# Kernel tuning notes

Hardware: AMD Instinct MI355X
Metric: run time of the kernel (lower is better)

Reference implementation:

```python
import jax, jax.numpy as jnp
import numpy as np
from jax import lax

# dims (see shape_source)
B, C, H, W = 2, 128, 48, 48
HEADS = 4
G = 4                 # offset_groups = heads
DH = C // HEADS       # 32, dim_head
DF = 4                # downsample_factor
OKS = 6               # offset_kernel_size
PAD = (OKS - DF) // 2 # 1
OFFSET_SCALE = 4.0
CPB_DIM = C // 4      # 32
OD = C // G           # offset_dims = 32


def setup_inputs() -> dict:
    key = jax.random.key(0)
    ks = jax.random.split(key, 12)
    rn = lambda k, shape, s=0.05: jax.random.normal(k, shape, dtype=jnp.float32) * s
    return {
        "x": jax.random.normal(ks[0], (B, C, H, W), dtype=jnp.float32),
        "gamma": jax.random.normal(ks[1], (1,), dtype=jnp.float32),  # nn.Parameter([0.0]); randomized so both paths contribute
        "wq": rn(ks[2], (G, DH, C // G)),    # grouped 1x1 conv, groups=G
        "wk": rn(ks[3], (G, DH, C // G)),
        "wv": rn(ks[4], (G, DH, C // G)),
        "wo": rn(ks[5], (C, C)),             # to_out 1x1 conv
        "bo": jnp.zeros((C,), jnp.float32),
        "w_off_dw": rn(ks[6], (OD, 1, OKS, OKS)),  # depthwise conv k=6 s=4 p=1
        "b_off_dw": jnp.zeros((OD,), jnp.float32),
        "w_off_proj": rn(ks[7], (2, OD)),          # 1x1 conv to 2 offset channels, no bias
        "cpb_w0": rn(ks[8], (2, CPB_DIM), 0.5),
        "cpb_b0": jnp.zeros((CPB_DIM,), jnp.float32),
        "cpb_w1": rn(ks[9], (CPB_DIM, CPB_DIM), 0.2),
        "cpb_b1": jnp.zeros((CPB_DIM,), jnp.float32),
        "cpb_w2": rn(ks[10], (CPB_DIM, HEADS // G), 0.2),
        "cpb_b2": jnp.zeros((HEADS // G,), jnp.float32),
    }


def _bilinear_sample(img, px, py):
    """F.grid_sample(mode='bilinear', padding_mode='zeros') on pixel coords.
    img: (N, Cg, Hi, Wi); px, py: (N, Ho, Wo) -> (N, Cg, Ho, Wo)"""
    N, Cg, Hi, Wi = img.shape
    imgf = img.reshape(N, Cg, Hi * Wi)
    x0 = jnp.floor(px)
    y0 = jnp.floor(py)
    wx1 = px - x0
    wy1 = py - y0

    def corner(xc, yc, w):
        valid = (xc >= 0) & (xc <= Wi - 1) & (yc >= 0) & (yc <= Hi - 1)
        xi = jnp.clip(xc, 0, Wi - 1).astype(jnp.int32)
        yi = jnp.clip(yc, 0, Hi - 1).astype(jnp.int32)
        idx = (yi * Wi + xi).reshape(N, -1)
        vals = jnp.take_along_axis(imgf, idx[:, None, :], axis=2)  # (N,Cg,Ho*Wo)
        return vals * (w * valid).reshape(N, 1, -1)

    out = (corner(x0, y0, (1 - wx1) * (1 - wy1))
           + corner(x0 + 1, y0, wx1 * (1 - wy1))
           + corner(x0, y0 + 1, (1 - wx1) * wy1)
           + corner(x0 + 1, y0 + 1, wx1 * wy1))
    return out.reshape(N, Cg, px.shape[1], px.shape[2])


def _forward(x, gamma, wq, wk, wv, wo, bo, w_off_dw, b_off_dw, w_off_proj,
             cpb_w0, cpb_b0, cpb_w1, cpb_b1, cpb_w2, cpb_b2):
    b = x.shape[0]
    scale = DH ** -0.5
    xg = x.reshape(b, G, C // G, H, W)
    # grouped 1x1 conv -> queries (b, G, DH, H, W); channel layout (g d) == (h d) since G==HEADS
    q = jnp.einsum('bgchw,goc->bgohw', xg, wq)
    gq = q.reshape(b * G, DH, H, W)
    # to_offsets: depthwise conv (k=6, s=4, p=1) -> GELU -> 1x1 to 2ch -> tanh -> *offset_scale
    off = lax.conv_general_dilated(gq, w_off_dw, (DF, DF), [(PAD, PAD), (PAD, PAD)],
                                   feature_group_count=OD,
                                   dimension_numbers=('NCHW', 'OIHW', 'NCHW'))
    off = jax.nn.gelu(off + b_off_dw[None, :, None, None], approximate=False)
    off = jnp.tanh(jnp.einsum('bchw,oc->bohw', off, w_off_proj)) * OFFSET_SCALE  # (bG,2,Hd,Wd)
    Hd, Wd = off.shape[-2], off.shape[-1]
    gy, gx = jnp.meshgrid(jnp.arange(Hd, dtype=jnp.float32),
                          jnp.arange(Wd, dtype=jnp.float32), indexing='ij')
    vg0 = gx[None] + off[:, 0]  # channel 0 = x (meshgrid 'xy' in torch code)
    vg1 = gy[None] + off[:, 1]  # channel 1 = y
    vn0 = 2.0 * vg0 / max(Hd - 1, 1) - 1.0  # normalize_grid (H==W so h/w quirk is moot)
    vn1 = 2.0 * vg1 / max(Wd - 1, 1) - 1.0
    # grid_sample align_corners=False unnormalization: pix = ((u+1)*size - 1)/2
    px = ((vn0 + 1.0) * W - 1.0) / 2.0
    py = ((vn1 + 1.0) * H - 1.0) / 2.0
    kv = _bilinear_sample(xg.reshape(b * G, C // G, H, W), px, py)  # (bG, C/G, Hd, Wd)
    kvg = kv.reshape(b, G, C // G, Hd, Wd)
    k = jnp.einsum('bgchw,goc->bgohw', kvg, wk)
    v = jnp.einsum('bgchw,goc->bgohw', kvg, wv)
    i, j = H * W, Hd * Wd
    qh = q.reshape(b, HEADS, DH, i).transpose(0, 1, 3, 2) * scale  # (b,h,i,d)
    kh = k.reshape(b, HEADS, DH, j).transpose(0, 1, 3, 2)
    vh = v.reshape(b, HEADS, DH, j).transpose(0, 1, 3, 2)
    sim = jnp.einsum('bhid,bhjd->bhij', qh, kh)
    # CPB relative position bias
    gyq, gxq = jnp.meshgrid(jnp.arange(H, dtype=jnp.float32),
                            jnp.arange(W, dtype=jnp.float32), indexing='ij')
    qn0 = 2.0 * gxq / max(H - 1, 1) - 1.0
    qn1 = 2.0 * gyq / max(W - 1, 1) - 1.0
    grid_q = jnp.stack([qn0, qn1], -1).reshape(1, i, 1, 2)
    grid_kv = jnp.stack([vn0, vn1], -1).reshape(b * G, 1, j, 2)
    pos = grid_q - grid_kv                       # (bG, i, j, 2)
    bias = jnp.sign(pos) * jnp.log1p(jnp.abs(pos))
    h1 = jax.nn.relu(bias @ cpb_w0 + cpb_b0)
    h2 = jax.nn.relu(h1 @ cpb_w1 + cpb_b1)
    bias = h2 @ cpb_w2 + cpb_b2                  # (bG, i, j, heads//G)
    bias = bias.reshape(b, G, i, j, HEADS // G).transpose(0, 1, 4, 2, 3).reshape(b, HEADS, i, j)
    attn = jax.nn.softmax(sim + bias, axis=-1)
    outh = jnp.einsum('bhij,bhjd->bhid', attn, vh)
    out = outh.transpose(0, 1, 3, 2).reshape(b, C, H, W)  # 'b h (x y) d -> b (h d) x y'
    attention = jnp.einsum('bchw,oc->bohw', out, wo) + bo[None, :, None, None]
    return gamma[0] * attention + x, attention


def reference(x, gamma, wq, wk, wv, wo, bo, w_off_dw, b_off_dw, w_off_proj,
              cpb_w0, cpb_b0, cpb_w1, cpb_b1, cpb_w2, cpb_b2):
    return _forward(x, gamma, wq, wk, wv, wo, bo, w_off_dw, b_off_dw, w_off_proj,
                    cpb_w0, cpb_b0, cpb_w1, cpb_b1, cpb_w2, cpb_b2)
```

## Files before the change

### kernel.cpp

```cpp
#include <hip/hip_runtime.h>
#include <math.h>

#define HWHW 2304
#define JD   144
#define LSP  148

typedef __attribute__((ext_vector_type(8))) short short8;
typedef __attribute__((ext_vector_type(4))) float f32x4;

__device__ inline ushort f2bf(float f) {
  uint u = __float_as_uint(f);
  u += 0x7fffu + ((u >> 16) & 1u);
  return (ushort)(u >> 16);
}
__device__ inline float bf2f(ushort s) { return __uint_as_float((uint)s << 16); }


__global__ __launch_bounds__(256) void qproj_kernel(
    const float* __restrict__ x, const float* __restrict__ wq,
    ushort* __restrict__ qt) {
  int hw = blockIdx.x * 256 + threadIdx.x;
  int o0 = blockIdx.y * 8, bg = blockIdx.z;
  int b = bg >> 2, g = bg & 3;
  const float* xp = x + (b * 128 + g * 32) * HWHW + hw;
  float xv[32];
#pragma unroll
  for (int c = 0; c < 32; ++c) xv[c] = xp[c * HWHW];
  uint p[4];
#pragma unroll
  for (int oo = 0; oo < 8; oo += 2) {
    const float* w0r = wq + (g * 32 + o0 + oo) * 32;
    const float* w1r = wq + (g * 32 + o0 + oo + 1) * 32;
    float a0 = 0.f, a1 = 0.f;
#pragma unroll
    for (int c = 0; c < 32; ++c) { a0 += w0r[c] * xv[c]; a1 += w1r[c] * xv[c]; }
    p[oo >> 1] = (uint)f2bf(a0) | ((uint)f2bf(a1) << 16);
  }
  *(uint4*)(qt + ((long)bg * HWHW + hw) * 32 + o0) = make_uint4(p[0], p[1], p[2], p[3]);
}

__global__ __launch_bounds__(384) void offset_kv_kernel(
    const ushort* __restrict__ qt, const float* __restrict__ wdw,
    const float* __restrict__ bdw, const float* __restrict__ wproj,
    const float* __restrict__ x, const float* __restrict__ wk,
    const float* __restrict__ wv,
    float* __restrict__ vn0, float* __restrict__ vn1,
    ushort* __restrict__ ktb, ushort* __restrict__ vtb) {
  __shared__ float qs[288][32];
  __shared__ float wdws[36][32];
  __shared__ float wkl[32][33], wvl[32][33];
  __shared__ float kvs[32][13];
  __shared__ float spx[12], spy[12];
  int hd = blockIdx.x, bg = blockIdx.y, b = bg >> 2, g = bg & 3;
  int t = threadIdx.x;
  for (int u = t; u < 4608; u += 384) {
    int r = u >> 4, c2 = u & 15;
    int ry = r / 48, col = r - ry * 48;
    int hy = hd * 4 - 1 + ry;
    uint v = 0;
    if (hy >= 0 && hy < 48)
      v = ((const uint*)qt)[((long)bg * HWHW + hy * 48 + col) * 16 + c2];
    qs[r][c2 * 2] = bf2f((ushort)v);
    qs[r][c2 * 2 + 1] = bf2f((ushort)(v >> 16));
  }
  for (int u = t; u < 1152; u += 384) wdws[u >> 5][u & 31] = wdw[(u & 31) * 36 + (u >> 5)];
  for (int u = t; u < 1024; u += 384) {
    int d = u >> 5, c = u & 31;
    wkl[d][c] = wk[g * 1024 + u];
    wvl[d][c] = wv[g * 1024 + u];
  }
  __syncthreads();
  {
    int wd = t >> 5, c = t & 31;
    float s = 0.f;
#pragma unroll
    for (int ky = 0; ky < 6; ++ky) {
#pragma unroll
      for (int kx = 0; kx < 6; ++kx) {
        int wx = wd * 4 - 1 + kx;
        if (wx >= 0 && wx < 48)
          s += wdws[ky * 6 + kx][c] * qs[ky * 48 + wx][c];
      }
    }
    s += bdw[c];
    s = 0.5f * s * (1.f + erff(s * 0.70710678118654752f));
    float g0 = wproj[c] * s;
    float g1 = wproj[32 + c] * s;
#pragma unroll
    for (int k = 16; k >= 1; k >>= 1) {
      g0 += __shfl_xor(g0, k, 64);
      g1 += __shfl_xor(g1, k, 64);
    }
    if (c == 0) {
      float off0 = tanhf(g0) * 4.f;
      float off1 = tanhf(g1) * 4.f;
      float n0 = 2.f * ((float)wd + off0) / 11.f - 1.f;
      float n1 = 2.f * ((float)hd + off1) / 11.f - 1.f;
      int idx = bg * JD + hd * 12 + wd;
      vn0[idx] = n0;
      vn1[idx] = n1;
      spx[wd] = ((n0 + 1.f) * 48.f - 1.f) * 0.5f;
      spy[wd] = ((n1 + 1.f) * 48.f - 1.f) * 0.5f;
    }
  }
  __syncthreads();
  {
    int j = t >> 5, c = t & 31;
    float fx = spx[j], fy = spy[j];
    float x0 = floorf(fx), y0 = floorf(fy);
    float wx = fx - x0, wy = fy - y0;
    int xi = (int)x0, yi = (int)y0;
    const float* xp = x + (b * 128 + g * 32 + c) * HWHW;
    float v00 = 0.f, v10 = 0.f, v01 = 0.f, v11 = 0.f;
    bool okx0 = (xi >= 0) & (xi < 48), okx1 = (xi + 1 >= 0) & (xi + 1 < 48);
    if (yi >= 0 && yi < 48) {
      if (okx0) v00 = xp[yi * 48 + xi];
      if (okx1) v10 = xp[yi * 48 + xi + 1];
    }
    if (yi + 1 >= 0 && yi + 1 < 48) {
      if (okx0) v01 = xp[(yi + 1) * 48 + xi];
      if (okx1) v11 = xp[(yi + 1) * 48 + xi + 1];
    }
    kvs[c][j] = v00 * (1.f - wx) * (1.f - wy) + v10 * wx * (1.f - wy)
              + v01 * (1.f - wx) * wy + v11 * wx * wy;
  }
  __syncthreads();
  {
    int j = t >> 5, d = t & 31;
    float ak = 0.f, av = 0.f;
#pragma unroll
    for (int c = 0; c < 32; ++c) {
      float val = kvs[c][j];
      ak += wkl[d][c] * val;
      av += wvl[d][c] * val;
    }
    int jg = hd * 12 + j;
    ktb[bg * 4608 + jg * 32 + d] = f2bf(ak);
    vtb[bg * 5120 + d * 160 + jg] = f2bf(av);
  }
  if (hd == 0) {
    for (int u = t; u < 512; u += 384)
      vtb[bg * 5120 + (u >> 4) * 160 + 144 + (u & 15)] = 0;
  }
}

__global__ __launch_bounds__(256) void attn_fused_kernel(
    const ushort* __restrict__ qt, const ushort* __restrict__ ktb,
    const ushort* __restrict__ vtb,
    const float* __restrict__ vn0, const float* __restrict__ vn1,
    const float* __restrict__ w0, const float* __restrict__ b0,
    const float* __restrict__ w1, const float* __restrict__ b1,
    const float* __restrict__ w2, const float* __restrict__ b2,
    ushort* __restrict__ outh) {
  __shared__ __align__(16) char smem[21888];
  float* Ls = (float*)smem;
  ushort* kbf = (ushort*)(smem + 9472);
  ushort* vbfT = (ushort*)(smem + 9472);
  ushort* qbf = (ushort*)(smem + 19712);
  float* sv0 = (float*)(smem + 20736);
  float* sv1 = (float*)(smem + 21312);

  int bg = blockIdx.y, b = bg >> 2, g = bg & 3;
  int i0 = blockIdx.x * 16;
  int t = threadIdx.x;
  int w = t >> 6, lane = t & 63;
  int lam = lane & 15, quad = lane >> 4;

  {
    const uint4* src = (const uint4*)(ktb + bg * 4608);
    uint4* dst = (uint4*)kbf;
    for (int u = t; u < 576; u += 256) dst[u] = src[u];
    if (t < 128) ((uint4*)qbf)[t & 127] =
        ((const uint4*)(qt + ((long)bg * HWHW + i0) * 32))[t & 127];
  }
  if (t < JD) { sv0[t] = vn0[bg * JD + t]; sv1[t] = vn1[bg * JD + t]; }

  float w00r[8], w01r[8], b0r[8];
#pragma unroll
  for (int j = 0; j < 8; ++j) {
    int k = quad * 8 + j;
    w00r[j] = w0[k]; w01r[j] = w0[32 + k]; b0r[j] = b0[k];
  }
  short8 w1f0, w1f1;
#pragma unroll
  for (int j = 0; j < 8; ++j) {
    int k = quad * 8 + j;
    w1f0[j] = (short)f2bf(w1[k * 32 + lam]);
    w1f1[j] = (short)f2bf(w1[k * 32 + 16 + lam]);
  }
  f32x4 zA, zB;
  float w2r[8];
#pragma unroll
  for (int r = 0; r < 4; ++r) {
    zA[r] = b1[quad * 4 + r];
    zB[r] = b1[16 + quad * 4 + r];
    w2r[r] = w2[quad * 4 + r];
    w2r[4 + r] = w2[16 + quad * 4 + r];
  }
  float b2s = b2[0];

  __syncthreads();

  const float scale = 0.17677669529663687f;
  {
    short8 aq = *(const short8*)(qbf + lam * 32 + quad * 8);
#pragma unroll 1
    for (int jt = w; jt < 9; jt += 4) {
      short8 bk = *(const short8*)(kbf + (jt * 16 + lam) * 32 + quad * 8);
      f32x4 acc = {0.f, 0.f, 0.f, 0.f};
      acc = __builtin_amdgcn_mfma_f32_16x16x32_bf16(aq, bk, acc, 0, 0, 0);
#pragma unroll
      for (int r = 0; r < 4; ++r)
        Ls[(quad * 4 + r) * LSP + jt * 16 + lam] = acc[r] * scale;
    }
  }
  __syncthreads();

#pragma unroll 1
  for (int s = 0; s < 9; ++s) {
    int P = s * 64 + lane;
    int ii = P / 144, jj = P - ii * 144;
    int ig = i0 + w * 4 + ii;
    int iy = ig / 48, ix = ig - iy * 48;
    float p0 = (float)ix * (2.f / 47.f) - 1.f - sv0[jj];
    float p1 = (float)iy * (2.f / 47.f) - 1.f - sv1[jj];
    float s0f = copysignf(__logf(1.f + fabsf(p0)), p0);
    float s1f = copysignf(__logf(1.f + fabsf(p1)), p1);
    float bm[4];
#pragma unroll
    for (int mt = 0; mt < 4; ++mt) {
      float s0 = __shfl(s0f, mt * 16 + lam, 64);
      float s1 = __shfl(s1f, mt * 16 + lam, 64);
      float h[8];
#pragma unroll
      for (int j = 0; j < 8; ++j)
        h[j] = fmaxf(fmaf(s0, w00r[j], fmaf(s1, w01r[j], b0r[j])), 0.f);
      union { uint u[4]; short8 s8; } cvt;
#pragma unroll
      for (int j = 0; j < 4; ++j)
        cvt.u[j] = __builtin_amdgcn_perm(__float_as_uint(h[2 * j + 1]),
                                         __float_as_uint(h[2 * j]), 0x07060302);
      f32x4 dA = __builtin_amdgcn_mfma_f32_16x16x32_bf16(w1f0, cvt.s8, zA, 0, 0, 0);
      f32x4 dB = __builtin_amdgcn_mfma_f32_16x16x32_bf16(w1f1, cvt.s8, zB, 0, 0, 0);
      float acc = 0.f;
#pragma unroll
      for (int r = 0; r < 4; ++r) {
        acc = fmaf(fmaxf(dA[r], 0.f), w2r[r], acc);
        acc = fmaf(fmaxf(dB[r], 0.f), w2r[4 + r], acc);
      }
      acc += __shfl_xor(acc, 16, 64);
      acc += __shfl_xor(acc, 32, 64);
      bm[mt] = acc;
    }
    float biasv = (quad == 0 ? bm[0] : quad == 1 ? bm[1] : quad == 2 ? bm[2] : bm[3]) + b2s;
    Ls[(w * 4 + ii) * LSP + jj] += biasv;
  }
  __syncthreads();

  {
    const uint4* src = (const uint4*)(vtb + bg * 5120);
    uint4* dst = (uint4*)vbfT;
    for (int u = t; u < 640; u += 256) dst[u] = src[u];
  }

#pragma unroll 1
  for (int rr = 0; rr < 4; ++rr) {
    int row = w * 4 + rr;
    const float* Lp = Ls + row * LSP;
    float l0 = Lp[lane], l1 = Lp[64 + lane];
    float l2 = (lane < 16) ? Lp[128 + lane] : -INFINITY;
    float m = fmaxf(fmaxf(l0, l1), l2);
#pragma unroll
    for (int k = 32; k >= 1; k >>= 1) m = fmaxf(m, __shfl_xor(m, k, 64));
    float e0 = __expf(l0 - m), e1 = __expf(l1 - m);
    float e2 = (lane < 16) ? __expf(l2 - m) : 0.f;
    float sum = e0 + e1 + e2;
#pragma unroll
    for (int k = 32; k >= 1; k >>= 1) sum += __shfl_xor(sum, k, 64);
    float inv = 1.f / sum;
    ushort* pb = (ushort*)(Lp + 64);
    pb[lane] = f2bf(e0 * inv);
    pb[64 + lane] = f2bf(e1 * inv);
    if (lane < 32) pb[128 + lane] = (lane < 16) ? f2bf(e2 * inv) : (ushort)0;
  }
  __syncthreads();

  if (w < 2) {
    f32x4 o = {0.f, 0.f, 0.f, 0.f};
    const ushort* pb = (const ushort*)(Ls + lam * LSP + 64);
    const ushort* vb = vbfT + (w * 16 + lam) * 160;
#pragma unroll
    for (int kb = 0; kb < 5; ++kb) {
      short8 ap = *(const short8*)(pb + kb * 32 + quad * 8);
      short8 bv = *(const short8*)(vb + kb * 32 + quad * 8);
      o = __builtin_amdgcn_mfma_f32_16x16x32_bf16(ap, bv, o, 0, 0, 0);
    }
#pragma unroll
    for (int r = 0; r < 4; ++r) {
      int ig = i0 + quad * 4 + r;
      outh[((long)b * HWHW + ig) * 128 + g * 32 + w * 16 + lam] = f2bf(o[r]);
    }
  }
}

__global__ __launch_bounds__(256) void out_kernel(
    const ushort* __restrict__ outh, const float* __restrict__ wo,
    const float* __restrict__ bo, const float* __restrict__ x,
    const float* __restrict__ gamma, float* __restrict__ out) {
  __shared__ __align__(16) char smem[39168];
  ushort* wob = (ushort*)smem;
  ushort* aob = (ushort*)(smem + 34816);
  int b = blockIdx.y;
  int hw0 = blockIdx.x * 16;
  int t = threadIdx.x;
  int w = t >> 6, lane = t & 63, lam = lane & 15, quad = lane >> 4;
  {
    const float2* wsrc = (const float2*)wo;
    for (int u = t; u < 8192; u += 256) {
      float2 v = wsrc[u];
      ((uint*)wob)[(u >> 6) * 68 + (u & 63)] =
          (uint)f2bf(v.x) | ((uint)f2bf(v.y) << 16);
    }
  }
  {
    const uint* src = (const uint*)(outh + ((long)b * HWHW + hw0) * 128);
    for (int u = t; u < 1024; u += 256)
      ((uint*)aob)[(u >> 6) * 68 + (u & 63)] = src[u];
  }
  __syncthreads();
  f32x4 acc0 = {0.f, 0.f, 0.f, 0.f}, acc1 = {0.f, 0.f, 0.f, 0.f};
#pragma unroll
  for (int ks = 0; ks < 4; ++ks) {
    short8 a = *(const short8*)(aob + lam * 136 + ks * 32 + quad * 8);
    short8 b0f = *(const short8*)(wob + (w * 32 + lam) * 136 + ks * 32 + quad * 8);
    short8 b1f = *(const short8*)(wob + (w * 32 + 16 + lam) * 136 + ks * 32 + quad * 8);
    acc0 = __builtin_amdgcn_mfma_f32_16x16x32_bf16(a, b0f, acc0, 0, 0, 0);
    acc1 = __builtin_amdgcn_mfma_f32_16x16x32_bf16(a, b1f, acc1, 0, 0, 0);
  }
  float gm = gamma[0];
  float* out0 = out;
  float* out1 = out + 2 * 128 * HWHW;
#pragma unroll
  for (int nt = 0; nt < 2; ++nt) {
    f32x4 acc = nt ? acc1 : acc0;
    int oc = w * 32 + nt * 16 + lam;
    float bv = bo[oc];
    long base = ((long)(b * 128 + oc)) * HWHW + hw0 + quad * 4;
    float4 xv = *(const float4*)(x + base);
    float4 a1, a0;
    a1.x = acc[0] + bv; a1.y = acc[1] + bv; a1.z = acc[2] + bv; a1.w = acc[3] + bv;
    a0.x = fmaf(gm, a1.x, xv.x); a0.y = fmaf(gm, a1.y, xv.y);
    a0.z = fmaf(gm, a1.z, xv.z); a0.w = fmaf(gm, a1.w, xv.w);
    *(float4*)(out1 + base) = a1;
    *(float4*)(out0 + base) = a0;
  }
}

extern "C" void kernel_launch(void* const* d_in, const int* in_sizes, int n_in,
                              void* d_out, int out_size, void* d_ws, size_t ws_size,
                              hipStream_t stream) {
  const float* x     = (const float*)d_in[0];
  const float* gamma = (const float*)d_in[1];
  const float* wq    = (const float*)d_in[2];
  const float* wk    = (const float*)d_in[3];
  const float* wv    = (const float*)d_in[4];
  const float* wo    = (const float*)d_in[5];
  const float* bo    = (const float*)d_in[6];
  const float* wdw   = (const float*)d_in[7];
  const float* bdw   = (const float*)d_in[8];
  const float* wproj = (const float*)d_in[9];
  const float* cw0   = (const float*)d_in[10];
  const float* cb0   = (const float*)d_in[11];
  const float* cw1   = (const float*)d_in[12];
  const float* cb1   = (const float*)d_in[13];
  const float* cw2   = (const float*)d_in[14];
  const float* cb2   = (const float*)d_in[15];
  char* wsb = (char*)d_ws;
  ushort* qt  = (ushort*)wsb;
  float* vn0  = (float*)(wsb + 1179648);
  float* vn1  = (float*)(wsb + 1184256);
  ushort* ktb = (ushort*)(wsb + 1188864);
  ushort* vtb = (ushort*)(wsb + 1262592);
  ushort* outh = (ushort*)(wsb + 1344512);
  float* out  = (float*)d_out;

  qproj_kernel<<<dim3(9, 4, 8), 256, 0, stream>>>(x, wq, qt);
  offset_kv_kernel<<<dim3(12, 8), 384, 0, stream>>>(qt, wdw, bdw, wproj, x, wk, wv,
                                                    vn0, vn1, ktb, vtb);
  attn_fused_kernel<<<dim3(144, 8), 256, 0, stream>>>(qt, ktb, vtb, vn0, vn1,
                                                      cw0, cb0, cw1, cb1, cw2, cb2, outh);
  out_kernel<<<dim3(144, 2), 256, 0, stream>>>(outh, wo, bo, x, gamma, out);
}
```

Before: 138.0 us.

## Load MFMA operands directly from global memory instead of staging in LDS

The attention kernel no longer copies Q, K and V tiles into shared memory. It reads the MFMA fragments straight from global memory, which shrinks its LDS footprint and drops one barrier. The output projection kernel drops its shared-memory staging of the full wo matrix and the activation tile. It now loads fp32 weights per fragment and packs them to bf16 by truncation instead of round-to-nearest. This removes the redundant per-block conversion and copy of wo and should raise occupancy, at the cost of more uncoalesced global and L2 reads and a small rounding change.

Result: no change. 135.6 us (-1.7%).

```diff
diff --git a/kernel.cpp b/kernel.cpp
--- a/kernel.cpp
+++ b/kernel.cpp
@@ -14,6 +14,9 @@
   return (ushort)(u >> 16);
 }
 __device__ inline float bf2f(ushort s) { return __uint_as_float((uint)s << 16); }
+__device__ inline uint packbf(float hi, float lo) {
+  return __builtin_amdgcn_perm(__float_as_uint(hi), __float_as_uint(lo), 0x07060302);
+}
 
 
 __global__ __launch_bounds__(256) void qproj_kernel(
@@ -152,13 +155,10 @@
     const float* __restrict__ w1, const float* __restrict__ b1,
     const float* __restrict__ w2, const float* __restrict__ b2,
     ushort* __restrict__ outh) {
-  __shared__ __align__(16) char smem[21888];
+  __shared__ __align__(16) char smem[10624];
   float* Ls = (float*)smem;
-  ushort* kbf = (ushort*)(smem + 9472);
-  ushort* vbfT = (ushort*)(smem + 9472);
-  ushort* qbf = (ushort*)(smem + 19712);
-  float* sv0 = (float*)(smem + 20736);
-  float* sv1 = (float*)(smem + 21312);
+  float* sv0 = (float*)(smem + 9472);
+  float* sv1 = (float*)(smem + 10048);
 
   int bg = blockIdx.y, b = bg >> 2, g = bg & 3;
   int i0 = blockIdx.x * 16;
@@ -166,13 +166,6 @@
   int w = t >> 6, lane = t & 63;
   int lam = lane & 15, quad = lane >> 4;
 
-  {
-    const uint4* src = (const uint4*)(ktb + bg * 4608);
-    uint4* dst = (uint4*)kbf;
-    for (int u = t; u < 576; u += 256) dst[u] = src[u];
-    if (t < 128) ((uint4*)qbf)[t & 127] =
-        ((const uint4*)(qt + ((long)bg * HWHW + i0) * 32))[t & 127];
-  }
   if (t < JD) { sv0[t] = vn0[bg * JD + t]; sv1[t] = vn1[bg * JD + t]; }
 
   float w00r[8], w01r[8], b0r[8];
@@ -199,14 +192,13 @@
   }
   float b2s = b2[0];
 
-  __syncthreads();
-
   const float scale = 0.17677669529663687f;
   {
-    short8 aq = *(const short8*)(qbf + lam * 32 + quad * 8);
+    short8 aq = *(const short8*)(qt + ((long)bg * HWHW + i0 + lam) * 32 + quad * 8);
+    const ushort* kb = ktb + bg * 4608;
 #pragma unroll 1
     for (int jt = w; jt < 9; jt += 4) {
-      short8 bk = *(const short8*)(kbf + (jt * 16 + lam) * 32 + quad * 8);
+      short8 bk = *(const short8*)(kb + (jt * 16 + lam) * 32 + quad * 8);
       f32x4 acc = {0.f, 0.f, 0.f, 0.f};
       acc = __builtin_amdgcn_mfma_f32_16x16x32_bf16(aq, bk, acc, 0, 0, 0);
 #pragma unroll
@@ -237,9 +229,7 @@
         h[j] = fmaxf(fmaf(s0, w00r[j], fmaf(s1, w01r[j], b0r[j])), 0.f);
       union { uint u[4]; short8 s8; } cvt;
 #pragma unroll
-      for (int j = 0; j < 4; ++j)
-        cvt.u[j] = __builtin_amdgcn_perm(__float_as_uint(h[2 * j + 1]),
-                                         __float_as_uint(h[2 * j]), 0x07060302);
+      for (int j = 0; j < 4; ++j) cvt.u[j] = packbf(h[2 * j + 1], h[2 * j]);
       f32x4 dA = __builtin_amdgcn_mfma_f32_16x16x32_bf16(w1f0, cvt.s8, zA, 0, 0, 0);
       f32x4 dB = __builtin_amdgcn_mfma_f32_16x16x32_bf16(w1f1, cvt.s8, zB, 0, 0, 0);
       float acc = 0.f;
@@ -257,12 +247,6 @@
   }
   __syncthreads();
 
-  {
-    const uint4* src = (const uint4*)(vtb + bg * 5120);
-    uint4* dst = (uint4*)vbfT;
-    for (int u = t; u < 640; u += 256) dst[u] = src[u];
-  }
-
 #pragma unroll 1
   for (int rr = 0; rr < 4; ++rr) {
     int row = w * 4 + rr;
@@ -288,7 +272,7 @@
   if (w < 2) {
     f32x4 o = {0.f, 0.f, 0.f, 0.f};
     const ushort* pb = (const ushort*)(Ls + lam * LSP + 64);
-    const ushort* vb = vbfT + (w * 16 + lam) * 160;
+    const ushort* vb = vtb + bg * 5120 + (w * 16 + lam) * 160;
 #pragma unroll
     for (int kb = 0; kb < 5; ++kb) {
       short8 ap = *(const short8*)(pb + kb * 32 + quad * 8);
@@ -307,35 +291,28 @@
     const ushort* __restrict__ outh, const float* __restrict__ wo,
     const float* __restrict__ bo, const float* __restrict__ x,
     const float* __restrict__ gamma, float* __restrict__ out) {
-  __shared__ __align__(16) char smem[39168];
-  ushort* wob = (ushort*)smem;
-  ushort* aob = (ushort*)(smem + 34816);
   int b = blockIdx.y;
   int hw0 = blockIdx.x * 16;
   int t = threadIdx.x;
   int w = t >> 6, lane = t & 63, lam = lane & 15, quad = lane >> 4;
-  {
-    const float2* wsrc = (const float2*)wo;
-    for (int u = t; u < 8192; u += 256) {
-      float2 v = wsrc[u];
-      ((uint*)wob)[(u >> 6) * 68 + (u & 63)] =
-          (uint)f2bf(v.x) | ((uint)f2bf(v.y) << 16);
-    }
-  }
-  {
-    const uint* src = (const uint*)(outh + ((long)b * HWHW + hw0) * 128);
-    for (int u = t; u < 1024; u += 256)
-      ((uint*)aob)[(u >> 6) * 68 + (u & 63)] = src[u];
-  }
-  __syncthreads();
+  const ushort* abase = outh + ((long)b * HWHW + hw0 + lam) * 128 + quad * 8;
+  const float* wb0 = wo + (w * 32 + lam) * 128 + quad * 8;
+  const float* wb1 = wo + (w * 32 + 16 + lam) * 128 + quad * 8;
   f32x4 acc0 = {0.f, 0.f, 0.f, 0.f}, acc1 = {0.f, 0.f, 0.f, 0.f};
 #pragma unroll
   for (int ks = 0; ks < 4; ++ks) {
-    short8 a = *(const short8*)(aob + lam * 136 + ks * 32 + quad * 8);
-    short8 b0f = *(const short8*)(wob + (w * 32 + lam) * 136 + ks * 32 + quad * 8);
-    short8 b1f = *(const short8*)(wob + (w * 32 + 16 + lam) * 136 + ks * 32 + quad * 8);
-    acc0 = __builtin_amdgcn_mfma_f32_16x16x32_bf16(a, b0f, acc0, 0, 0, 0);
-    acc1 = __builtin_amdgcn_mfma_f32_16x16x32_bf16(a, b1f, acc1, 0, 0, 0);
+    short8 a = *(const short8*)(abase + ks * 32);
+    float4 wa = *(const float4*)(wb0 + ks * 32);
+    float4 wb = *(const float4*)(wb0 + ks * 32 + 4);
+    float4 wc = *(const float4*)(wb1 + ks * 32);
+    float4 wd = *(const float4*)(wb1 + ks * 32 + 4);
+    union { uint u[4]; short8 s8; } p0, p1;
+    p0.u[0] = packbf(wa.y, wa.x); p0.u[1] = packbf(wa.w, wa.z);
+    p0.u[2] = packbf(wb.y, wb.x); p0.u[3] = packbf(wb.w, wb.z);
+    p1.u[0] = packbf(wc.y, wc.x); p1.u[1] = packbf(wc.w, wc.z);
+    p1.u[2] = packbf(wd.y, wd.x); p1.u[3] = packbf(wd.w, wd.z);
+    acc0 = __builtin_amdgcn_mfma_f32_16x16x32_bf16(a, p0.s8, acc0, 0, 0, 0);
+    acc1 = __builtin_amdgcn_mfma_f32_16x16x32_bf16(a, p1.s8, acc1, 0, 0, 0);
   }
   float gm = gamma[0];
   float* out0 = out;
```
